# Kernel tuning notes

Hardware: AMD Instinct MI355X
Metric: run time of the kernel (lower is better)

Reference implementation:

```python
import jax, jax.numpy as jnp
import numpy as np
import math

NUM_HEADS = 16
SEGMENT_SIZE = 128
DILATION = 2


def hilbert_map(seq_len: int) -> np.ndarray:
    """Boustrophedon ('Hilbert') permutation, matching the torch reference."""
    if seq_len <= 64:
        return np.arange(seq_len, dtype=np.int64)
    g = int(math.ceil(math.sqrt(seq_len)))
    fm = np.zeros(seq_len, dtype=np.int64)
    idx = 0
    for row in range(g):
        cols = range(g) if row % 2 == 0 else range(g - 1, -1, -1)
        for col in cols:
            lp = row * g + col
            if lp < seq_len and idx < seq_len:
                fm[lp] = idx
                idx += 1
    return fm


def setup_inputs() -> dict:
    key = jax.random.key(0)
    k1, k2, k3 = jax.random.split(key, 3)
    B, S, D = 2, 8192, 1024
    x = jax.random.normal(k1, (B, S, D), dtype=jnp.float32)
    W_qkv = jax.random.normal(k2, (D, 3 * D), dtype=jnp.float32) * 0.02
    W_out = jax.random.normal(k3, (D, D), dtype=jnp.float32) * 0.02
    return {"x": x, "W_qkv": W_qkv, "W_out": W_out}


def reference(x, W_qkv, W_out):
    B, S, Dm = x.shape
    H, Dh = NUM_HEADS, Dm // NUM_HEADS
    seg, dil = SEGMENT_SIZE, DILATION
    scale = Dh ** -0.5

    qkv = (x @ W_qkv).reshape(B, S, 3, H, Dh)
    q = jnp.transpose(qkv[:, :, 0], (0, 2, 1, 3))  # [B,H,S,Dh]
    k = jnp.transpose(qkv[:, :, 1], (0, 2, 1, 3))
    v = jnp.transpose(qkv[:, :, 2], (0, 2, 1, 3))

    # Hilbert reorder (active since S > 64)
    m = jnp.asarray(hilbert_map(S))
    q, k, v = q[:, :, m], k[:, :, m], v[:, :, m]

    # Vectorized segment-local dilated attention (S % seg == 0 here)
    nseg = S // seg
    qs = q.reshape(B, H, nseg, seg, Dh)
    ks = k.reshape(B, H, nseg, seg, Dh)[:, :, :, ::dil]  # dilated keys
    vs = v.reshape(B, H, nseg, seg, Dh)[:, :, :, ::dil]
    scores = jnp.einsum('bhnqd,bhnkd->bhnqk', qs, ks) * scale
    attn = jax.nn.softmax(scores, axis=-1)
    out = jnp.einsum('bhnqk,bhnkd->bhnqd', attn, vs).reshape(B, H, S, Dh)

    # Reverse Hilbert ordering
    inv = jnp.argsort(m)
    out = out[:, :, inv]

    out = jnp.transpose(out, (0, 2, 1, 3)).reshape(B, S, Dm)
    return out @ W_out
```

## Files before the change

kernel.cpp:

```cpp
#include <hip/hip_runtime.h>
#include <stdint.h>

typedef unsigned short ushort_t;
typedef __bf16 bf16x8 __attribute__((ext_vector_type(8)));
typedef float  f32x4  __attribute__((ext_vector_type(4)));

#define DEV static __device__ __forceinline__

DEV ushort_t f2bf(float f){
  union { float f; unsigned u; } x; x.f = f;
  unsigned u = x.u;
  return (ushort_t)((u + 0x7fffu + ((u >> 16) & 1u)) >> 16);
}

DEV int hmap(int p){
  int r = p / 91;
  int c = p - r * 91;
  return (r & 1) ? (r * 91 + 90 - c) : p;
}

DEV int arow_rt(int r, int gather){
  if (gather == 0) return r;
  if (gather == 1){ int b = r >> 13, p = r & 8191; return b * 8192 + hmap(p); }
  int b = r >> 12, rem = r & 4095, seg = rem >> 6, j = rem & 63;
  return b * 8192 + hmap(seg * 128 + 2 * j);
}

DEV void async16(const void* g, void* l){
  __builtin_amdgcn_global_load_lds(
      (const __attribute__((address_space(1))) unsigned*)g,
      (__attribute__((address_space(3))) unsigned*)l, 16, 0, 0);
}

__global__ __launch_bounds__(256) void prep_kernel(const float* __restrict__ x,
                                                   const float* __restrict__ Wqkv,
                                                   const float* __restrict__ Wout,
                                                   ushort_t* __restrict__ xb,
                                                   ushort_t* __restrict__ WqT,
                                                   ushort_t* __restrict__ WoT){
  __shared__ ushort_t t[64 * 66];
  int id = blockIdx.x, tid = threadIdx.x;
  if (id < 2048){
    const int n4 = (16384 * 1024) / 4;
    int stride = 2048 * 256;
    for (int i = id * 256 + tid; i < n4; i += stride){
      float4 v = ((const float4*)x)[i];
      ushort4 o;
      o.x = f2bf(v.x); o.y = f2bf(v.y); o.z = f2bf(v.z); o.w = f2bf(v.w);
      ((ushort4*)xb)[i] = o;
    }
    return;
  }
  const float* W; ushort_t* WT; int rows, cols, bx, by;
  if (id < 2816){ int q = id - 2048; W = Wqkv; WT = WqT; rows = 1024; cols = 3072; bx = q % 48; by = q / 48; }
  else          { int q = id - 2816; W = Wout; WT = WoT; rows = 1024; cols = 1024; bx = q % 16; by = q / 16; }
  int c0 = bx * 64, r0 = by * 64;
  int cl = tid & 63, rb = tid >> 6;
  for (int i = 0; i < 16; ++i){
    int r = rb + i * 4;
    t[r * 66 + cl] = f2bf(W[(size_t)(r0 + r) * cols + c0 + cl]);
  }
  __syncthreads();
  int rr = tid & 63, cb = tid >> 6;
  for (int i = 0; i < 16; ++i){
    int cc = cb + i * 4;
    WT[(size_t)(c0 + cc) * rows + r0 + rr] = t[rr * 66 + cc];
  }
}


#define BARRIER() asm volatile("s_barrier" ::: "memory")
#define VMCNT8()  asm volatile("s_waitcnt vmcnt(8)" ::: "memory")
#define VMCNT0()  asm volatile("s_waitcnt vmcnt(0)" ::: "memory")

#define STAGE_A_TO(DST, T1)                                                    \
  {                                                                            \
    _Pragma("unroll") for (int i = 0; i < 4; ++i)                              \
      async16(&A[asrcR[i] + (size_t)(T1) * 64], &DST[i * 4096 + tid * 8]);     \
  }

#define STAGE_B_TO(DST, T1)                                                    \
  {                                                                            \
    _Pragma("unroll") for (int i = 0; i < 4; ++i)                              \
      async16(&BT[bsrcR[i] + (size_t)(T1) * 64], &DST[i * 4096 + tid * 8]);    \
  }

#define COMPUTE(ABUF, BBUF)                                                    \
  {                                                                            \
    bf16x8 bv[4][2];                                                           \
    _Pragma("unroll") for (int ni = 0; ni < 4; ++ni)                           \
      _Pragma("unroll") for (int kk = 0; kk < 2; ++kk)                         \
        bv[ni][kk] = *(const bf16x8*)&BBUF[(wn * 64 + ni * 16 + md) * 64 + axor[kk]]; \
    _Pragma("unroll") for (int kk = 0; kk < 2; ++kk)                           \
      _Pragma("unroll") for (int mi = 0; mi < 8; ++mi){                        \
        bf16x8 af = *(const bf16x8*)&ABUF[(wm * 128 + mi * 16 + md) * 64 + axor[kk]]; \
        _Pragma("unroll") for (int ni = 0; ni < 4; ++ni)                       \
          acc[mi][ni] = __builtin_amdgcn_mfma_f32_16x16x32_bf16(               \
              af, bv[ni][kk], acc[mi][ni], 0, 0, 0);                           \
      }                                                                        \
  }

#define TILE_STEP(CUR, NXT, TSTAGE)                                            \
  {                                                                            \
    if ((TSTAGE) < NT){                                                        \
      STAGE_A_TO(As##NXT, TSTAGE); STAGE_B_TO(Bs##NXT, TSTAGE);                \
      VMCNT8();                                                                \
    } else { VMCNT0(); }                                                       \
    BARRIER();                                                                 \
    COMPUTE(As##CUR, Bs##CUR);                                                 \
    BARRIER();                                                                 \
  }

template<int OUT_BF16>
DEV void gemm_body(const ushort_t* __restrict__ A, const ushort_t* __restrict__ BT,
                   void* __restrict__ Cout, int N, int K, int gather, int m0, int n0,
                   ushort_t* As0, ushort_t* As1, ushort_t* Bs0, ushort_t* Bs1){
  const int NT = K >> 6;
  int tid = threadIdx.x;
  int lane = tid & 63, w = tid >> 6;
  int md = lane & 15, qd = lane >> 4;
  int wm = w >> 2, wn = w & 3;

  int rbase = tid >> 3;
  int g0 = ((tid & 7) ^ (rbase & 7)) * 8;
  size_t asrcR[4], bsrcR[4];
  #pragma unroll
  for (int i = 0; i < 4; ++i){
    asrcR[i] = (size_t)arow_rt(m0 + i * 64 + rbase, gather) * K + g0;
    bsrcR[i] = (size_t)(n0 + i * 64 + rbase) * K + g0;
  }

  int axor[2] = { (qd ^ (md & 7)) * 8, ((4 + qd) ^ (md & 7)) * 8 };

  f32x4 acc[8][4];
  #pragma unroll
  for (int a = 0; a < 8; ++a)
    #pragma unroll
    for (int b = 0; b < 4; ++b)
      #pragma unroll
      for (int e = 0; e < 4; ++e) acc[a][b][e] = 0.f;

  STAGE_A_TO(As0, 0);
  STAGE_B_TO(Bs0, 0);
  VMCNT0(); BARRIER();

  for (int t = 0; t < NT; t += 2){
    TILE_STEP(0, 1, t + 1);
    TILE_STEP(1, 0, t + 2);
  }

  if (OUT_BF16){
    float* wbuf = (w < 4) ? ((float*)As0 + w * 1040) : ((float*)As1 + (w - 4) * 1040);
    int r16 = lane >> 4, c16 = lane & 15;
    #pragma unroll
    for (int mi = 0; mi < 8; ++mi){
      #pragma unroll
      for (int ni = 0; ni < 4; ++ni)
        #pragma unroll
        for (int reg = 0; reg < 4; ++reg)
          wbuf[(qd * 4 + reg) * 65 + ni * 16 + md] = acc[mi][ni][reg];
      #pragma unroll
      for (int rr = 0; rr < 4; ++rr){
        int row = rr * 4 + r16;
        float4 v = *(const float4*)&wbuf[row * 65 + c16 * 4];
        int grow = m0 + wm * 128 + mi * 16 + row;
        int gcol = n0 + wn * 64 + c16 * 4;
        ushort4 ob;
        ob.x = f2bf(v.x); ob.y = f2bf(v.y); ob.z = f2bf(v.z); ob.w = f2bf(v.w);
        *(ushort4*)&((ushort_t*)Cout)[(size_t)grow * N + gcol] = ob;
      }
    }
  } else {
    #pragma unroll
    for (int mi = 0; mi < 8; ++mi)
      #pragma unroll
      for (int ni = 0; ni < 4; ++ni){
        f32x4 v = acc[mi][ni];
        #pragma unroll
        for (int reg = 0; reg < 4; ++reg){
          int grow = m0 + wm * 128 + mi * 16 + qd * 4 + reg;
          int gcol = n0 + wn * 64 + ni * 16 + md;
          ((float*)Cout)[(size_t)grow * N + gcol] = v[reg];
        }
      }
  }
}

__global__ __launch_bounds__(512, 2) void gemm_qkv(const ushort_t* __restrict__ xb,
                                                   const ushort_t* __restrict__ WqT,
                                                   ushort_t* __restrict__ Qbuf,
                                                   ushort_t* __restrict__ KVbuf){
  __shared__ __align__(16) ushort_t As0[16384];
  __shared__ __align__(16) ushort_t As1[16384];
  __shared__ __align__(16) ushort_t Bs0[16384];
  __shared__ __align__(16) ushort_t Bs1[16384];
  int id = blockIdx.x;
  const ushort_t* BT; ushort_t* C; int N, gather, m0, n0;
  if (id < 256){
    int o = id;
    m0 = (o & 63) << 8; n0 = (o >> 6) << 8;
    BT = WqT; C = Qbuf; N = 1024; gather = 1;
  } else {
    int o = id - 256;
    m0 = (o & 31) << 8; n0 = (o >> 5) << 8;
    BT = WqT + (size_t)1024 * 1024; C = KVbuf; N = 2048; gather = 2;
  }
  gemm_body<1>(xb, BT, C, N, 1024, gather, m0, n0, As0, As1, Bs0, Bs1);
}

__global__ __launch_bounds__(512, 2) void gemm_out(const ushort_t* __restrict__ aoutb,
                                                   const ushort_t* __restrict__ WoT,
                                                   float* __restrict__ out){
  __shared__ __align__(16) ushort_t As0[16384];
  __shared__ __align__(16) ushort_t As1[16384];
  __shared__ __align__(16) ushort_t Bs0[16384];
  __shared__ __align__(16) ushort_t Bs1[16384];
  int o = blockIdx.x;
  int m0 = (o & 63) << 8, n0 = (o >> 6) << 8;
  gemm_body<0>(aoutb, WoT, out, 1024, 1024, 0, m0, n0, As0, As1, Bs0, Bs1);
}

__global__ __launch_bounds__(256) void attn_kernel(const ushort_t* __restrict__ Qb,
                                                   const ushort_t* __restrict__ KV,
                                                   ushort_t* __restrict__ aout){
  __shared__ ushort_t Qs[128 * 72];
  __shared__ ushort_t Ks[64 * 72];
  __shared__ ushort_t Vt[64 * 72];
  int tid  = threadIdx.x;
  int lane = tid & 63, w = tid >> 6;
  int qd = lane >> 4, md = lane & 15;
  int seg = blockIdx.x, h = blockIdx.y, b = blockIdx.z;
  int p0 = seg * 128;

  for (int it = 0; it < 4; ++it){
    int q = it * 256 + tid;
    int r = q >> 3, ch = q & 7;
    uint4 d = *(const uint4*)&Qb[(size_t)(b * 8192 + p0 + r) * 1024 + h * 64 + ch * 8];
    *(uint4*)&Qs[r * 72 + ch * 8] = d;
  }
  for (int it = 0; it < 2; ++it){
    int q = it * 256 + tid;
    int r = q >> 3, ch = q & 7;
    uint4 d = *(const uint4*)&KV[(size_t)(b * 4096 + seg * 64 + r) * 2048 + h * 64 + ch * 8];
    *(uint4*)&Ks[r * 72 + ch * 8] = d;
  }
  for (int it = 0; it < 2; ++it){
    int q = it * 256 + tid;
    int r = q >> 3, ch = q & 7;
    union { uint4 v; ushort_t u[8]; } d;
    d.v = *(const uint4*)&KV[(size_t)(b * 4096 + seg * 64 + r) * 2048 + 1024 + h * 64 + ch * 8];
    int kslot = ((r >> 3) ^ ch) * 8 + (r & 7);
    for (int e = 0; e < 8; ++e) Vt[(ch * 8 + e) * 72 + kslot] = d.u[e];
  }
  __syncthreads();

  f32x4 z = {0.f, 0.f, 0.f, 0.f};
  f32x4 sc[2][4];
  for (int mi = 0; mi < 2; ++mi) for (int ni = 0; ni < 4; ++ni) sc[mi][ni] = z;
  for (int kc = 0; kc < 2; ++kc){
    bf16x8 aq[2], bk[4];
    for (int mi = 0; mi < 2; ++mi)
      aq[mi] = *(const bf16x8*)&Qs[(w * 32 + mi * 16 + md) * 72 + kc * 32 + qd * 8];
    for (int ni = 0; ni < 4; ++ni)
      bk[ni] = *(const bf16x8*)&Ks[(ni * 16 + md) * 72 + kc * 32 + qd * 8];
    for (int mi = 0; mi < 2; ++mi)
      for (int ni = 0; ni < 4; ++ni)
        sc[mi][ni] = __builtin_amdgcn_mfma_f32_16x16x32_bf16(aq[mi], bk[ni], sc[mi][ni], 0, 0, 0);
  }

  const float scale = 0.125f;
  ushort_t* Ps = Qs;
  for (int mi = 0; mi < 2; ++mi){
    for (int i = 0; i < 4; ++i){
      float mx = sc[mi][0][i];
      for (int ni = 1; ni < 4; ++ni) mx = fmaxf(mx, sc[mi][ni][i]);
      for (int d = 1; d < 16; d <<= 1) mx = fmaxf(mx, __shfl_xor(mx, d));
      float e[4], sum = 0.f;
      for (int ni = 0; ni < 4; ++ni){ e[ni] = __expf((sc[mi][ni][i] - mx) * scale); sum += e[ni]; }
      for (int d = 1; d < 16; d <<= 1) sum += __shfl_xor(sum, d);
      float inv = 1.0f / sum;
      int r = w * 32 + mi * 16 + qd * 4 + i;
      for (int ni = 0; ni < 4; ++ni)
        Ps[r * 72 + ni * 16 + md] = f2bf(e[ni] * inv);
    }
  }

  f32x4 oc[2][4];
  for (int mi = 0; mi < 2; ++mi) for (int ni = 0; ni < 4; ++ni) oc[mi][ni] = z;
  for (int kc = 0; kc < 2; ++kc){
    bf16x8 ap[2], bv[4];
    for (int mi = 0; mi < 2; ++mi)
      ap[mi] = *(const bf16x8*)&Ps[(w * 32 + mi * 16 + md) * 72 + kc * 32 + qd * 8];
    for (int ni = 0; ni < 4; ++ni){
      int dd = ni * 16 + md;
      int vchunk = ((kc * 4 + qd) ^ ((dd >> 3) & 7)) & 7;
      bv[ni] = *(const bf16x8*)&Vt[dd * 72 + vchunk * 8];
    }
    for (int mi = 0; mi < 2; ++mi)
      for (int ni = 0; ni < 4; ++ni)
        oc[mi][ni] = __builtin_amdgcn_mfma_f32_16x16x32_bf16(ap[mi], bv[ni], oc[mi][ni], 0, 0, 0);
  }

  for (int mi = 0; mi < 2; ++mi){
    for (int i = 0; i < 4; ++i){
      int rl = w * 32 + mi * 16 + qd * 4 + i;
      for (int ni = 0; ni < 4; ++ni)
        Ps[rl * 72 + ni * 16 + md] = f2bf(oc[mi][ni][i]);
    }
  }
  __syncthreads();
  for (int it = 0; it < 4; ++it){
    int q = it * 256 + tid;
    int r = q >> 3, ch = q & 7;
    int s = hmap(p0 + r);
    *(uint4*)&aout[(size_t)(b * 8192 + s) * 1024 + h * 64 + ch * 8] =
        *(const uint4*)&Qs[r * 72 + ch * 8];
  }
}

extern "C" void kernel_launch(void* const* d_in, const int* in_sizes, int n_in,
                              void* d_out, int out_size, void* d_ws, size_t ws_size,
                              hipStream_t stream){
  const float* x    = (const float*)d_in[0];
  const float* Wqkv = (const float*)d_in[1];
  const float* Wout = (const float*)d_in[2];
  float* out = (float*)d_out;

  char* ws = (char*)d_ws;
  ushort_t* xb    = (ushort_t*)(ws);
  ushort_t* WqT   = (ushort_t*)(ws + 33554432);
  ushort_t* WoT   = (ushort_t*)(ws + 39845888);
  ushort_t* Qbuf  = (ushort_t*)(ws + 41943040);
  ushort_t* KVbuf = (ushort_t*)(ws + 75497472);
  ushort_t* aoutb = (ushort_t*)(ws + 109051904);

  prep_kernel<<<3072, 256, 0, stream>>>(x, Wqkv, Wout, xb, WqT, WoT);
  gemm_qkv<<<512, 512, 0, stream>>>(xb, WqT, Qbuf, KVbuf);
  attn_kernel<<<dim3(64, 16, 2), 256, 0, stream>>>(Qbuf, KVbuf, aoutb);
  gemm_out<<<256, 512, 0, stream>>>(aoutb, WoT, out);
}
```

Measured before the change: 267.3 us.

## Stage attention Q/K via async LDS loads with XOR swizzle; vectorize fp32 GEMM epilogue

In the attention kernel, Q and K tiles are now loaded straight from global into LDS with global_load_lds. Because that path cannot pad rows, the LDS layout changes from padded rows to an XOR-swizzled 64-wide layout, and every Q/K/P/output access is remapped to match. The fp32 output GEMM epilogue now goes through the same LDS staging as the bf16 path and writes float4 instead of scattered scalar stores, and the staging pitch changes from 65 to 68. The goals are fewer register round trips when loading and coalesced output writes, at the cost of one extra LDS pass in the fp32 epilogue. There is no explicit vmcnt wait before the __syncthreads, so whether the async loads have landed in LDS depends on how the compiler lowers the barrier.

```diff
diff --git a/kernel.cpp b/kernel.cpp
--- a/kernel.cpp
+++ b/kernel.cpp
@@ -30,6 +30,10 @@
   __builtin_amdgcn_global_load_lds(
       (const __attribute__((address_space(1))) unsigned*)g,
       (__attribute__((address_space(3))) unsigned*)l, 16, 0, 0);
+}
+
+DEV int sw64(int r, int c){
+  return r * 64 + (((c >> 3) ^ (r & 7)) << 3) + (c & 7);
 }
 
 __global__ __launch_bounds__(256) void prep_kernel(const float* __restrict__ x,
@@ -149,40 +153,29 @@
     TILE_STEP(1, 0, t + 2);
   }
 
-  if (OUT_BF16){
-    float* wbuf = (w < 4) ? ((float*)As0 + w * 1040) : ((float*)As1 + (w - 4) * 1040);
-    int r16 = lane >> 4, c16 = lane & 15;
+  float* wbuf = (float*)((w < 4) ? (void*)As0 : (void*)As1) + (w & 3) * 1088;
+  int r16 = lane >> 4, c16 = lane & 15;
+  #pragma unroll
+  for (int mi = 0; mi < 8; ++mi){
     #pragma unroll
-    for (int mi = 0; mi < 8; ++mi){
+    for (int ni = 0; ni < 4; ++ni)
       #pragma unroll
-      for (int ni = 0; ni < 4; ++ni)
-        #pragma unroll
-        for (int reg = 0; reg < 4; ++reg)
-          wbuf[(qd * 4 + reg) * 65 + ni * 16 + md] = acc[mi][ni][reg];
-      #pragma unroll
-      for (int rr = 0; rr < 4; ++rr){
-        int row = rr * 4 + r16;
-        float4 v = *(const float4*)&wbuf[row * 65 + c16 * 4];
-        int grow = m0 + wm * 128 + mi * 16 + row;
-        int gcol = n0 + wn * 64 + c16 * 4;
+      for (int reg = 0; reg < 4; ++reg)
+        wbuf[(qd * 4 + reg) * 68 + ni * 16 + md] = acc[mi][ni][reg];
+    #pragma unroll
+    for (int rr = 0; rr < 4; ++rr){
+      int row = rr * 4 + r16;
+      float4 v = *(const float4*)&wbuf[row * 68 + c16 * 4];
+      int grow = m0 + wm * 128 + mi * 16 + row;
+      int gcol = n0 + wn * 64 + c16 * 4;
+      if (OUT_BF16){
         ushort4 ob;
         ob.x = f2bf(v.x); ob.y = f2bf(v.y); ob.z = f2bf(v.z); ob.w = f2bf(v.w);
         *(ushort4*)&((ushort_t*)Cout)[(size_t)grow * N + gcol] = ob;
+      } else {
+        *(float4*)&((float*)Cout)[(size_t)grow * N + gcol] = v;
       }
     }
-  } else {
-    #pragma unroll
-    for (int mi = 0; mi < 8; ++mi)
-      #pragma unroll
-      for (int ni = 0; ni < 4; ++ni){
-        f32x4 v = acc[mi][ni];
-        #pragma unroll
-        for (int reg = 0; reg < 4; ++reg){
-          int grow = m0 + wm * 128 + mi * 16 + qd * 4 + reg;
-          int gcol = n0 + wn * 64 + ni * 16 + md;
-          ((float*)Cout)[(size_t)grow * N + gcol] = v[reg];
-        }
-      }
   }
 }
 
@@ -223,8 +216,8 @@
 __global__ __launch_bounds__(256) void attn_kernel(const ushort_t* __restrict__ Qb,
                                                    const ushort_t* __restrict__ KV,
                                                    ushort_t* __restrict__ aout){
-  __shared__ ushort_t Qs[128 * 72];
-  __shared__ ushort_t Ks[64 * 72];
+  __shared__ __align__(16) ushort_t Qs[128 * 64];
+  __shared__ __align__(16) ushort_t Ks[64 * 64];
   __shared__ ushort_t Vt[64 * 72];
   int tid  = threadIdx.x;
   int lane = tid & 63, w = tid >> 6;
@@ -232,24 +225,25 @@
   int seg = blockIdx.x, h = blockIdx.y, b = blockIdx.z;
   int p0 = seg * 128;
 
+  #pragma unroll
   for (int it = 0; it < 4; ++it){
-    int q = it * 256 + tid;
-    int r = q >> 3, ch = q & 7;
-    uint4 d = *(const uint4*)&Qb[(size_t)(b * 8192 + p0 + r) * 1024 + h * 64 + ch * 8];
-    *(uint4*)&Qs[r * 72 + ch * 8] = d;
-  }
+    int q = it * 256 + tid, r = q >> 3, ch = q & 7;
+    async16(&Qb[(size_t)(b * 8192 + p0 + r) * 1024 + h * 64 + ((ch ^ (r & 7)) << 3)],
+            &Qs[q * 8]);
+  }
+  #pragma unroll
   for (int it = 0; it < 2; ++it){
-    int q = it * 256 + tid;
-    int r = q >> 3, ch = q & 7;
-    uint4 d = *(const uint4*)&KV[(size_t)(b * 4096 + seg * 64 + r) * 2048 + h * 64 + ch * 8];
-    *(uint4*)&Ks[r * 72 + ch * 8] = d;
-  }
+    int q = it * 256 + tid, r = q >> 3, ch = q & 7;
+    async16(&KV[(size_t)(b * 4096 + seg * 64 + r) * 2048 + h * 64 + ((ch ^ (r & 7)) << 3)],
+            &Ks[q * 8]);
+  }
+  #pragma unroll
   for (int it = 0; it < 2; ++it){
-    int q = it * 256 + tid;
-    int r = q >> 3, ch = q & 7;
+    int q = it * 256 + tid, r = q >> 3, ch = q & 7;
     union { uint4 v; ushort_t u[8]; } d;
     d.v = *(const uint4*)&KV[(size_t)(b * 4096 + seg * 64 + r) * 2048 + 1024 + h * 64 + ch * 8];
     int kslot = ((r >> 3) ^ ch) * 8 + (r & 7);
+    #pragma unroll
     for (int e = 0; e < 8; ++e) Vt[(ch * 8 + e) * 72 + kslot] = d.u[e];
   }
   __syncthreads();
@@ -260,9 +254,9 @@
   for (int kc = 0; kc < 2; ++kc){
     bf16x8 aq[2], bk[4];
     for (int mi = 0; mi < 2; ++mi)
-      aq[mi] = *(const bf16x8*)&Qs[(w * 32 + mi * 16 + md) * 72 + kc * 32 + qd * 8];
+      aq[mi] = *(const bf16x8*)&Qs[sw64(w * 32 + mi * 16 + md, kc * 32 + qd * 8)];
     for (int ni = 0; ni < 4; ++ni)
-      bk[ni] = *(const bf16x8*)&Ks[(ni * 16 + md) * 72 + kc * 32 + qd * 8];
+      bk[ni] = *(const bf16x8*)&Ks[sw64(ni * 16 + md, kc * 32 + qd * 8)];
     for (int mi = 0; mi < 2; ++mi)
       for (int ni = 0; ni < 4; ++ni)
         sc[mi][ni] = __builtin_amdgcn_mfma_f32_16x16x32_bf16(aq[mi], bk[ni], sc[mi][ni], 0, 0, 0);
@@ -281,7 +275,7 @@
       float inv = 1.0f / sum;
       int r = w * 32 + mi * 16 + qd * 4 + i;
       for (int ni = 0; ni < 4; ++ni)
-        Ps[r * 72 + ni * 16 + md] = f2bf(e[ni] * inv);
+        Ps[sw64(r, ni * 16 + md)] = f2bf(e[ni] * inv);
     }
   }
 
@@ -290,7 +284,7 @@
   for (int kc = 0; kc < 2; ++kc){
     bf16x8 ap[2], bv[4];
     for (int mi = 0; mi < 2; ++mi)
-      ap[mi] = *(const bf16x8*)&Ps[(w * 32 + mi * 16 + md) * 72 + kc * 32 + qd * 8];
+      ap[mi] = *(const bf16x8*)&Ps[sw64(w * 32 + mi * 16 + md, kc * 32 + qd * 8)];
     for (int ni = 0; ni < 4; ++ni){
       int dd = ni * 16 + md;
       int vchunk = ((kc * 4 + qd) ^ ((dd >> 3) & 7)) & 7;
@@ -305,7 +299,7 @@
     for (int i = 0; i < 4; ++i){
       int rl = w * 32 + mi * 16 + qd * 4 + i;
       for (int ni = 0; ni < 4; ++ni)
-        Ps[rl * 72 + ni * 16 + md] = f2bf(oc[mi][ni][i]);
+        Ps[sw64(rl, ni * 16 + md)] = f2bf(oc[mi][ni][i]);
     }
   }
   __syncthreads();
@@ -314,7 +308,7 @@
     int r = q >> 3, ch = q & 7;
     int s = hmap(p0 + r);
     *(uint4*)&aout[(size_t)(b * 8192 + s) * 1024 + h * 64 + ch * 8] =
-        *(const uint4*)&Qs[r * 72 + ch * 8];
+        *(const uint4*)&Qs[sw64(r, ch * 8)];
   }
 }
 
```

Result: no change. 268.4 us (+0.4%).
